# Kernel tuning notes

Measured on AMD Instinct MI355X. Metric: run time of the kernel, lower is better.

Reference implementation:

```python
import jax, jax.numpy as jnp
import numpy as np

N_EMBD = 256
B, T = 2, 512


def setup_inputs() -> dict:
    key = jax.random.key(0)
    kx, ks, kv = jax.random.split(key, 3)
    x = jax.random.normal(kx, (B, T, N_EMBD), dtype=jnp.float32)
    # init std 0.02 per nn.init.normal_(..., std=0.02); keeps I - scaled well-conditioned
    skew_param = 0.02 * jax.random.normal(ks, (N_EMBD, N_EMBD), dtype=jnp.float32)
    vector = 0.02 * jax.random.normal(kv, (1, N_EMBD), dtype=jnp.float32)
    return {"x": x, "skew_param": skew_param, "vector": vector}


def reference(x, skew_param, vector):
    n = skew_param.shape[0]
    skew = skew_param - skew_param.T                      # (n, n), skew-symmetric
    # scaled[b,t,i,j] = x[b,t,i] * skew[i,j]  -> (B, T, n, n)
    scaled = x[..., :, None] * skew
    eye = jnp.eye(n, dtype=x.dtype)
    # Cayley transform: (I - scaled)^{-1} (I + scaled), batched over (B, T)
    q = jnp.linalg.solve(eye - scaled, eye + scaled)      # (B, T, n, n)
    # (1, n) @ (B, T, n, n) -> (B, T, n) after squeezing the row dim
    out = jnp.einsum('n,btnm->btm', vector[0], q)
    return out
```

## Files before the change

kernel.cpp:

```cpp
#include <hip/hip_runtime.h>
#include <math.h>

#define N 256
#define G 4
#define BLK 512
#define S1 6
#define S2 3
#define SLS 10
#define SP1 11
#define VS 268
#define UTS 280
#define ZS 260
#define RIDGE 3e-5f

typedef _Float16 half8v __attribute__((ext_vector_type(8)));
typedef _Float16 half2v __attribute__((ext_vector_type(2)));
typedef float float4v __attribute__((ext_vector_type(4)));
typedef float float2v __attribute__((ext_vector_type(2)));

#define OFF_K     0
#define OFF_UT0   47168
#define OFF_UT1   49408
#define OFF_ZTW   51648
#define OFF_GRAM  55808
#define OFF_L     57744
#define OFF_D     59344
#define ARENA_SZ  59504

#define LD_FRAG(base, t) (*(const half8v*)((base) + (mn & 3) * UTS + 32 * (t) + 8 * mq))

#define MATVEC(basep, d0, d1) do {                                                          \
    float4v ma00_ = {0.f,0.f,0.f,0.f}, ma01_ = {0.f,0.f,0.f,0.f};                           \
    float4v ma10_ = {0.f,0.f,0.f,0.f}, ma11_ = {0.f,0.f,0.f,0.f};                           \
    _Pragma("unroll")                                                                       \
    for (int t_ = 0; t_ < 4; ++t_) {                                                        \
        half8v mb0_ = LD_FRAG(basep, t_);                                                   \
        half8v mb1_ = LD_FRAG(basep, t_ + 4);                                               \
        ma00_ = __builtin_amdgcn_mfma_f32_16x16x32_f16(Shi[t_],      mb0_, ma00_, 0, 0, 0); \
        ma01_ = __builtin_amdgcn_mfma_f32_16x16x32_f16(Shi[t_ + 4],  mb1_, ma01_, 0, 0, 0); \
        ma10_ = __builtin_amdgcn_mfma_f32_16x16x32_f16(Shi[8 + t_],  mb0_, ma10_, 0, 0, 0); \
        ma11_ = __builtin_amdgcn_mfma_f32_16x16x32_f16(Shi[12 + t_], mb1_, ma11_, 0, 0, 0); \
    }                                                                                       \
    float4v mz0_ = ma00_ + ma01_, mz1_ = ma10_ + ma11_;                                     \
    if (mn < 4) {                                                                           \
        *(float4v*)(zTw + mn * ZS + 32 * wv + 4 * mq) = mz0_;                               \
        *(float4v*)(zTw + mn * ZS + 32 * wv + 16 + 4 * mq) = mz1_;                          \
    }                                                                                       \
    float2v mzz_ = *(const float2v*)(zTw + g * ZS + c0);                                    \
    d0 = mzz_.x; d1 = mzz_.y;                                                               \
} while (0)

__global__ __launch_bounds__(BLK, 2) void cayley_v22(const float* __restrict__ x_all,
                                                     const float* __restrict__ P,
                                                     const float* __restrict__ v_in,
                                                     float* __restrict__ out, int batch) {
    __shared__ __align__(16) char arena[ARENA_SZ];
    float* sK      = (float*)(arena + OFF_K);
    _Float16* uT0  = (_Float16*)(arena + OFF_UT0);
    _Float16* uT1  = (_Float16*)(arena + OFF_UT1);
    float* zTw     = (float*)(arena + OFF_ZTW);
    float* sGram   = (float*)(arena + OFF_GRAM);
    float* sL      = (float*)(arena + OFF_L);
    float* sD      = (float*)(arena + OFF_D);

    const int tid = threadIdx.x;
    const int lane = tid & 63, wv = tid >> 6;
    const int mn = lane & 15, mq = lane >> 4;
    const int g = tid & 3;
    const int c0 = (tid >> 2) * 2;
    const int sys = blockIdx.x * G + g;
    const bool alive = sys < batch;

    half8v Shi[16];
#pragma unroll
    for (int p = 0; p < 2; ++p) {
        const int r = 32 * wv + 16 * p + mn;
#pragma unroll
        for (int t = 0; t < 8; ++t) {
            const int k0 = 32 * t + 8 * mq;
            float4v pa = *(const float4v*)(P + r * N + k0);
            float4v pb = *(const float4v*)(P + r * N + k0 + 4);
            half8v hi;
            hi[0] = (_Float16)(pa.x - P[(k0 + 0) * N + r]);
            hi[1] = (_Float16)(pa.y - P[(k0 + 1) * N + r]);
            hi[2] = (_Float16)(pa.z - P[(k0 + 2) * N + r]);
            hi[3] = (_Float16)(pa.w - P[(k0 + 3) * N + r]);
            hi[4] = (_Float16)(pb.x - P[(k0 + 4) * N + r]);
            hi[5] = (_Float16)(pb.y - P[(k0 + 5) * N + r]);
            hi[6] = (_Float16)(pb.z - P[(k0 + 6) * N + r]);
            hi[7] = (_Float16)(pb.w - P[(k0 + 7) * N + r]);
            Shi[p * 8 + t] = hi;
        }
    }

    float2v x2 = {0.f, 0.f};
    if (alive) x2 = *(const float2v*)(x_all + sys * N + c0);
    const float2v v2 = *(const float2v*)(v_in + c0);
    float w0 = 0.f, w1 = 0.f;

    for (int sw = 0; sw < 2; ++sw) {
        const int s = sw ? S2 : S1;

        float k0v, k1v;
        if (sw == 0) {
            k0v = alive ? v2.x : 0.f;
            k1v = alive ? v2.y : 0.f;
        } else {
            half2v h;
            h[0] = (_Float16)(x2.x * w0); h[1] = (_Float16)(x2.y * w1);
            *(half2v*)(uT1 + g * UTS + c0) = h;
            __syncthreads();
            float z0, z1;
            MATVEC(uT1, z0, z1);
            k0v = alive ? (v2.x - w0 - z0) : 0.f;
            k1v = alive ? (v2.y - w1 - z1) : 0.f;
        }
        {
            float2v k2 = {k0v, k1v};
            *(float2v*)(sK + g * VS + c0) = k2;
            half2v h;
            h[0] = (_Float16)(x2.x * k0v); h[1] = (_Float16)(x2.y * k1v);
            *(half2v*)(uT0 + g * UTS + c0) = h;
        }
        __syncthreads();

        for (int i = 1; i <= s; ++i) {
            float z0, z1;
            if (i & 1) { MATVEC(uT0, z0, z1); } else { MATVEC(uT1, z0, z1); }
            k0v = 0.5f * z0; k1v = 0.5f * z1;
            float2v k2 = {k0v, k1v};
            *(float2v*)(sK + (i * G + g) * VS + c0) = k2;
            if (i < s) {
                _Float16* dst = (i & 1) ? uT1 : uT0;
                half2v h;
                h[0] = (_Float16)(x2.x * k0v); h[1] = (_Float16)(x2.y * k1v);
                *(half2v*)(dst + g * UTS + c0) = h;
            }
            __syncthreads();
        }

        const int NP = (s + 1) * (s + 2) / 2;
        for (int pp = wv; pp < NP; pp += 8) {
            int i = 0, rem = pp;
            while (rem >= (s + 1 - i)) { rem -= (s + 1 - i); ++i; }
            const int j = i + rem;
            const int gq = lane >> 4, q = lane & 15;
            const float* ka = sK + (i * G + gq) * VS + 16 * q;
            const float* kb = sK + (j * G + gq) * VS + 16 * q;
            float p;
            {
                float4v a0 = *(const float4v*)(ka);
                float4v b0 = *(const float4v*)(kb);
                float4v a1 = *(const float4v*)(ka + 4);
                float4v b1 = *(const float4v*)(kb + 4);
                p = a0.x * b0.x;
                p = fmaf(a0.y, b0.y, p); p = fmaf(a0.z, b0.z, p); p = fmaf(a0.w, b0.w, p);
                p = fmaf(a1.x, b1.x, p); p = fmaf(a1.y, b1.y, p);
                p = fmaf(a1.z, b1.z, p); p = fmaf(a1.w, b1.w, p);
            }
            {
                float4v a0 = *(const float4v*)(ka + 8);
                float4v b0 = *(const float4v*)(kb + 8);
                float4v a1 = *(const float4v*)(ka + 12);
                float4v b1 = *(const float4v*)(kb + 12);
                p = fmaf(a0.x, b0.x, p); p = fmaf(a0.y, b0.y, p);
                p = fmaf(a0.z, b0.z, p); p = fmaf(a0.w, b0.w, p);
                p = fmaf(a1.x, b1.x, p); p = fmaf(a1.y, b1.y, p);
                p = fmaf(a1.z, b1.z, p); p = fmaf(a1.w, b1.w, p);
            }
            p += __shfl_xor(p, 1); p += __shfl_xor(p, 2);
            p += __shfl_xor(p, 4); p += __shfl_xor(p, 8);
            if (q == 0) {
                sGram[(i * SP1 + j) * G + gq] = p;
                if (i != j) sGram[(j * SP1 + i) * G + gq] = p;
            }
        }
        __syncthreads();

        if (wv < 4) {
            const int gq = wv;
            const int rr = lane;
#define GG(i, j) sGram[((i) * SP1 + (j)) * G + gq]
            float invn_r = 0.f;
            if (rr < s) {
                const float Brr = GG(rr, rr) + 4.f * GG(rr, rr + 1)
                                + 4.f * GG(rr + 1, rr + 1);
                invn_r = (Brr > 1e-30f) ? (1.f / sqrtf(Brr)) : 0.f;
            }
            for (int k = 0; k < s; ++k) {
                const float invn_k = __shfl(invn_r, k);
                float a = 0.f;
                if (rr >= k && rr < s) {
                    if (rr == k) {
                        a = 1.f + RIDGE;
                    } else {
                        const float Brk = GG(rr, k) + 2.f * GG(rr, k + 1)
                                        + 2.f * GG(rr + 1, k) + 4.f * GG(rr + 1, k + 1);
                        a = Brk * invn_r * invn_k;
                    }
                    for (int m = 0; m < k; ++m)
                        a = fmaf(-sL[(rr * SLS + m) * G + gq],
                                 sL[(k * SLS + m) * G + gq], a);
                }
                float dk = __shfl(a, k);
                dk = fmaxf(dk, 0.5f * RIDGE);
                const float invd = 1.f / sqrtf(dk);
                if (rr >= k && rr < s) sL[(rr * SLS + k) * G + gq] = a * invd;
            }
            float trr = 0.f, acc = 0.f;
            const float rhs = (rr < s)
                ? (GG(rr, 0) + 2.f * GG(rr + 1, 0)) * invn_r : 0.f;
#undef GG
            for (int k = 0; k < s; ++k) {
                const float Lkk = sL[(k * SLS + k) * G + gq];
                float tk = (Lkk > 1e-20f) ? (rhs - acc) / Lkk : 0.f;
                tk = __shfl(tk, k);
                if (rr == k) trr = tk;
                if (rr > k && rr < s)
                    acc = fmaf(sL[(rr * SLS + k) * G + gq], tk, acc);
            }
            float crr = 0.f;
            acc = 0.f;
            for (int k = s - 1; k >= 0; --k) {
                const float Lkk = sL[(k * SLS + k) * G + gq];
                float ck = (Lkk > 1e-20f) ? (trr - acc) / Lkk : 0.f;
                ck = __shfl(ck, k);
                if (rr == k) crr = ck;
                if (rr < k) acc = fmaf(sL[(k * SLS + rr) * G + gq], ck, acc);
            }
            if (rr < s) sD[rr * G + gq] = crr * invn_r;
        }
        __syncthreads();

        for (int i = 0; i < s; ++i) {
            const float ci = sD[i * G + g];
            float2v k2 = *(const float2v*)(sK + (i * G + g) * VS + c0);
            w0 = fmaf(ci, k2.x, w0);
            w1 = fmaf(ci, k2.y, w1);
        }
        if (sw == 0) __syncthreads();
    }

    if (alive) {
        float2v o2 = {2.f * w0 - v2.x, 2.f * w1 - v2.y};
        *(float2v*)(out + sys * N + c0) = o2;
    }
}

extern "C" void kernel_launch(void* const* d_in, const int* in_sizes, int n_in,
                              void* d_out, int out_size, void* d_ws, size_t ws_size,
                              hipStream_t stream) {
    const float* x = (const float*)d_in[0];
    const float* P = (const float*)d_in[1];
    const float* v = (const float*)d_in[2];
    float* out = (float*)d_out;
    const int batch = in_sizes[0] / N;

    const int nblk = (batch + G - 1) / G;
    hipLaunchKernelGGL(cayley_v22, dim3(nblk), dim3(BLK), 0, stream, x, P, v, out, batch);
}
```

Measured before the change: 83.62 us.

## Halve systems per block to double block count, four row tiles per wave

Each block now handles 2 systems with 256 threads instead of 4 systems with 512 threads, so the grid has twice as many blocks. Each wave now covers 64 rows of the skew matrix and holds 32 fp16 fragments in registers, issuing 8 MFMA chains per step. The Gram computation is split across half-waves and the shared arena is halved. The aim is better occupancy and more parallelism across CUs for the small batch of 1024 systems. The cost is higher register pressure and more repeated loading of the skew matrix per system.

```diff
diff --git a/kernel.cpp b/kernel.cpp
--- a/kernel.cpp
+++ b/kernel.cpp
@@ -2,8 +2,8 @@
 #include <math.h>
 
 #define N 256
-#define G 4
-#define BLK 512
+#define G 2
+#define BLK 256
 #define S1 6
 #define S2 3
 #define SLS 10
@@ -19,38 +19,46 @@
 typedef float float2v __attribute__((ext_vector_type(2)));
 
 #define OFF_K     0
-#define OFF_UT0   47168
-#define OFF_UT1   49408
-#define OFF_ZTW   51648
-#define OFF_GRAM  55808
-#define OFF_L     57744
-#define OFF_D     59344
-#define ARENA_SZ  59504
-
-#define LD_FRAG(base, t) (*(const half8v*)((base) + (mn & 3) * UTS + 32 * (t) + 8 * mq))
-
-#define MATVEC(basep, d0, d1) do {                                                          \
-    float4v ma00_ = {0.f,0.f,0.f,0.f}, ma01_ = {0.f,0.f,0.f,0.f};                           \
-    float4v ma10_ = {0.f,0.f,0.f,0.f}, ma11_ = {0.f,0.f,0.f,0.f};                           \
-    _Pragma("unroll")                                                                       \
-    for (int t_ = 0; t_ < 4; ++t_) {                                                        \
-        half8v mb0_ = LD_FRAG(basep, t_);                                                   \
-        half8v mb1_ = LD_FRAG(basep, t_ + 4);                                               \
-        ma00_ = __builtin_amdgcn_mfma_f32_16x16x32_f16(Shi[t_],      mb0_, ma00_, 0, 0, 0); \
-        ma01_ = __builtin_amdgcn_mfma_f32_16x16x32_f16(Shi[t_ + 4],  mb1_, ma01_, 0, 0, 0); \
-        ma10_ = __builtin_amdgcn_mfma_f32_16x16x32_f16(Shi[8 + t_],  mb0_, ma10_, 0, 0, 0); \
-        ma11_ = __builtin_amdgcn_mfma_f32_16x16x32_f16(Shi[12 + t_], mb1_, ma11_, 0, 0, 0); \
-    }                                                                                       \
-    float4v mz0_ = ma00_ + ma01_, mz1_ = ma10_ + ma11_;                                     \
-    if (mn < 4) {                                                                           \
-        *(float4v*)(zTw + mn * ZS + 32 * wv + 4 * mq) = mz0_;                               \
-        *(float4v*)(zTw + mn * ZS + 32 * wv + 16 + 4 * mq) = mz1_;                          \
-    }                                                                                       \
-    float2v mzz_ = *(const float2v*)(zTw + g * ZS + c0);                                    \
-    d0 = mzz_.x; d1 = mzz_.y;                                                               \
+#define OFF_UT0   23584
+#define OFF_UT1   24704
+#define OFF_ZTW   25824
+#define OFF_GRAM  27904
+#define OFF_L     28880
+#define OFF_D     29680
+#define ARENA_SZ  29760
+
+#define LD_FRAG(base, t) (*(const half8v*)((base) + (mn & 1) * UTS + 32 * (t) + 8 * mq))
+
+#define MATVEC(basep, d0, d1) do {                                                            \
+    float4v p0a_ = {0.f,0.f,0.f,0.f}, p0b_ = {0.f,0.f,0.f,0.f};                               \
+    float4v p1a_ = {0.f,0.f,0.f,0.f}, p1b_ = {0.f,0.f,0.f,0.f};                               \
+    float4v p2a_ = {0.f,0.f,0.f,0.f}, p2b_ = {0.f,0.f,0.f,0.f};                               \
+    float4v p3a_ = {0.f,0.f,0.f,0.f}, p3b_ = {0.f,0.f,0.f,0.f};                               \
+    _Pragma("unroll")                                                                         \
+    for (int t_ = 0; t_ < 4; ++t_) {                                                          \
+        half8v mb0_ = LD_FRAG(basep, t_);                                                     \
+        half8v mb1_ = LD_FRAG(basep, t_ + 4);                                                 \
+        p0a_ = __builtin_amdgcn_mfma_f32_16x16x32_f16(Shi[t_],      mb0_, p0a_, 0, 0, 0);     \
+        p0b_ = __builtin_amdgcn_mfma_f32_16x16x32_f16(Shi[t_ + 4],  mb1_, p0b_, 0, 0, 0);     \
+        p1a_ = __builtin_amdgcn_mfma_f32_16x16x32_f16(Shi[8 + t_],  mb0_, p1a_, 0, 0, 0);     \
+        p1b_ = __builtin_amdgcn_mfma_f32_16x16x32_f16(Shi[12 + t_], mb1_, p1b_, 0, 0, 0);     \
+        p2a_ = __builtin_amdgcn_mfma_f32_16x16x32_f16(Shi[16 + t_], mb0_, p2a_, 0, 0, 0);     \
+        p2b_ = __builtin_amdgcn_mfma_f32_16x16x32_f16(Shi[20 + t_], mb1_, p2b_, 0, 0, 0);     \
+        p3a_ = __builtin_amdgcn_mfma_f32_16x16x32_f16(Shi[24 + t_], mb0_, p3a_, 0, 0, 0);     \
+        p3b_ = __builtin_amdgcn_mfma_f32_16x16x32_f16(Shi[28 + t_], mb1_, p3b_, 0, 0, 0);     \
+    }                                                                                         \
+    if (mn < 2) {                                                                             \
+        float* zb_ = zTw + mn * ZS + 64 * wv + 4 * mq;                                        \
+        *(float4v*)(zb_)      = p0a_ + p0b_;                                                  \
+        *(float4v*)(zb_ + 16) = p1a_ + p1b_;                                                  \
+        *(float4v*)(zb_ + 32) = p2a_ + p2b_;                                                  \
+        *(float4v*)(zb_ + 48) = p3a_ + p3b_;                                                  \
+    }                                                                                         \
+    float2v mzz_ = *(const float2v*)(zTw + g * ZS + c0);                                      \
+    d0 = mzz_.x; d1 = mzz_.y;                                                                 \
 } while (0)
 
-__global__ __launch_bounds__(BLK, 2) void cayley_v22(const float* __restrict__ x_all,
+__global__ __launch_bounds__(BLK, 2) void cayley_v24(const float* __restrict__ x_all,
                                                      const float* __restrict__ P,
                                                      const float* __restrict__ v_in,
                                                      float* __restrict__ out, int batch) {
@@ -66,15 +74,15 @@
     const int tid = threadIdx.x;
     const int lane = tid & 63, wv = tid >> 6;
     const int mn = lane & 15, mq = lane >> 4;
-    const int g = tid & 3;
-    const int c0 = (tid >> 2) * 2;
+    const int g = tid & 1;
+    const int c0 = (tid >> 1) * 2;
     const int sys = blockIdx.x * G + g;
     const bool alive = sys < batch;
 
-    half8v Shi[16];
+    half8v Shi[32];
 #pragma unroll
-    for (int p = 0; p < 2; ++p) {
-        const int r = 32 * wv + 16 * p + mn;
+    for (int p = 0; p < 4; ++p) {
+        const int r = 64 * wv + 16 * p + mn;
 #pragma unroll
         for (int t = 0; t < 8; ++t) {
             const int k0 = 32 * t + 8 * mq;
@@ -140,44 +148,48 @@
         }
 
         const int NP = (s + 1) * (s + 2) / 2;
-        for (int pp = wv; pp < NP; pp += 8) {
-            int i = 0, rem = pp;
-            while (rem >= (s + 1 - i)) { rem -= (s + 1 - i); ++i; }
-            const int j = i + rem;
-            const int gq = lane >> 4, q = lane & 15;
-            const float* ka = sK + (i * G + gq) * VS + 16 * q;
-            const float* kb = sK + (j * G + gq) * VS + 16 * q;
-            float p;
-            {
-                float4v a0 = *(const float4v*)(ka);
-                float4v b0 = *(const float4v*)(kb);
-                float4v a1 = *(const float4v*)(ka + 4);
-                float4v b1 = *(const float4v*)(kb + 4);
-                p = a0.x * b0.x;
-                p = fmaf(a0.y, b0.y, p); p = fmaf(a0.z, b0.z, p); p = fmaf(a0.w, b0.w, p);
-                p = fmaf(a1.x, b1.x, p); p = fmaf(a1.y, b1.y, p);
-                p = fmaf(a1.z, b1.z, p); p = fmaf(a1.w, b1.w, p);
-            }
-            {
-                float4v a0 = *(const float4v*)(ka + 8);
-                float4v b0 = *(const float4v*)(kb + 8);
-                float4v a1 = *(const float4v*)(ka + 12);
-                float4v b1 = *(const float4v*)(kb + 12);
-                p = fmaf(a0.x, b0.x, p); p = fmaf(a0.y, b0.y, p);
-                p = fmaf(a0.z, b0.z, p); p = fmaf(a0.w, b0.w, p);
-                p = fmaf(a1.x, b1.x, p); p = fmaf(a1.y, b1.y, p);
-                p = fmaf(a1.z, b1.z, p); p = fmaf(a1.w, b1.w, p);
-            }
-            p += __shfl_xor(p, 1); p += __shfl_xor(p, 2);
-            p += __shfl_xor(p, 4); p += __shfl_xor(p, 8);
-            if (q == 0) {
-                sGram[(i * SP1 + j) * G + gq] = p;
-                if (i != j) sGram[(j * SP1 + i) * G + gq] = p;
+        {
+            const int hf = lane >> 5;
+            const int q16 = lane & 15;
+            const int gq = (lane >> 4) & 1;
+            for (int pp = wv * 2 + hf; pp < NP; pp += 8) {
+                int i = 0, rem = pp;
+                while (rem >= (s + 1 - i)) { rem -= (s + 1 - i); ++i; }
+                const int j = i + rem;
+                const float* ka = sK + (i * G + gq) * VS + 16 * q16;
+                const float* kb = sK + (j * G + gq) * VS + 16 * q16;
+                float p;
+                {
+                    float4v a0 = *(const float4v*)(ka);
+                    float4v b0 = *(const float4v*)(kb);
+                    float4v a1 = *(const float4v*)(ka + 4);
+                    float4v b1 = *(const float4v*)(kb + 4);
+                    p = a0.x * b0.x;
+                    p = fmaf(a0.y, b0.y, p); p = fmaf(a0.z, b0.z, p); p = fmaf(a0.w, b0.w, p);
+                    p = fmaf(a1.x, b1.x, p); p = fmaf(a1.y, b1.y, p);
+                    p = fmaf(a1.z, b1.z, p); p = fmaf(a1.w, b1.w, p);
+                }
+                {
+                    float4v a0 = *(const float4v*)(ka + 8);
+                    float4v b0 = *(const float4v*)(kb + 8);
+                    float4v a1 = *(const float4v*)(ka + 12);
+                    float4v b1 = *(const float4v*)(kb + 12);
+                    p = fmaf(a0.x, b0.x, p); p = fmaf(a0.y, b0.y, p);
+                    p = fmaf(a0.z, b0.z, p); p = fmaf(a0.w, b0.w, p);
+                    p = fmaf(a1.x, b1.x, p); p = fmaf(a1.y, b1.y, p);
+                    p = fmaf(a1.z, b1.z, p); p = fmaf(a1.w, b1.w, p);
+                }
+                p += __shfl_xor(p, 1); p += __shfl_xor(p, 2);
+                p += __shfl_xor(p, 4); p += __shfl_xor(p, 8);
+                if (q16 == 0) {
+                    sGram[(i * SP1 + j) * G + gq] = p;
+                    if (i != j) sGram[(j * SP1 + i) * G + gq] = p;
+                }
             }
         }
         __syncthreads();
 
-        if (wv < 4) {
+        if (wv < G) {
             const int gq = wv;
             const int rr = lane;
 #define GG(i, j) sGram[((i) * SP1 + (j)) * G + gq]
@@ -257,5 +269,5 @@
     const int batch = in_sizes[0] / N;
 
     const int nblk = (batch + G - 1) / G;
-    hipLaunchKernelGGL(cayley_v22, dim3(nblk), dim3(BLK), 0, stream, x, P, v, out, batch);
+    hipLaunchKernelGGL(cayley_v24, dim3(nblk), dim3(BLK), 0, stream, x, P, v, out, batch);
 }
```

Result: slower. 169.3 us (+102.5%).
